# Kernel optimization log

Hardware: AMD Instinct MI355X
Metric: run time of the kernel (lower is better)

## Reference

```python
import jax, jax.numpy as jnp
import numpy as np

NUM_HEADS = 16
D_MODEL = 1024
DEPTH = D_MODEL // NUM_HEADS
THRESHOLD = 0.1
BATCH = 2
SEQ = 2048


def setup_inputs() -> dict:
    key = jax.random.key(0)
    ks = jax.random.split(key, 9)
    w_scale = 1.0 / np.sqrt(D_MODEL)
    Q = jax.random.normal(ks[0], (BATCH, SEQ, D_MODEL), dtype=jnp.float32)
    T = jax.random.normal(ks[1], (BATCH, SEQ, D_MODEL), dtype=jnp.float32)
    V = jax.random.normal(ks[2], (BATCH, SEQ, D_MODEL), dtype=jnp.float32)
    Wq = jax.random.normal(ks[3], (NUM_HEADS, D_MODEL, DEPTH), dtype=jnp.float32) * w_scale
    Wk = jax.random.normal(ks[4], (NUM_HEADS, D_MODEL, DEPTH), dtype=jnp.float32) * w_scale
    Wv = jax.random.normal(ks[5], (NUM_HEADS, D_MODEL, DEPTH), dtype=jnp.float32) * w_scale
    Wo = jax.random.normal(ks[6], (D_MODEL, D_MODEL), dtype=jnp.float32) * w_scale
    bq = jnp.zeros((NUM_HEADS, DEPTH), dtype=jnp.float32)
    bk = jnp.zeros((NUM_HEADS, DEPTH), dtype=jnp.float32)
    bv = jnp.zeros((NUM_HEADS, DEPTH), dtype=jnp.float32)
    bo = jnp.zeros((D_MODEL,), dtype=jnp.float32)
    return {"Q": Q, "T": T, "V": V, "Wq": Wq, "bq": bq, "Wk": Wk, "bk": bk,
            "Wv": Wv, "bv": bv, "Wo": Wo, "bo": bo}


def reference(Q, T, V, Wq, bq, Wk, bk, Wv, bv, Wo, bo):
    # Per-head projections (stacked over heads): [B,S,D] x [H,D,E] -> [B,H,S,E]
    q = jnp.einsum('bsd,hde->bhse', Q, Wq) + bq[None, :, None, :]
    k = jnp.einsum('bsd,hde->bhse', T, Wk) + bk[None, :, None, :]
    v = jnp.einsum('bsd,hde->bhse', V, Wv) + bv[None, :, None, :]

    # Raw scores (NOT pre-scaled): [B,H,S,S]
    scores = jnp.einsum('bhqe,bhke->bhqk', q, k)
    # tf.where(A>thr, A, -2**32 * cast(A>thr)) -> failing entries become 0
    scores = jnp.where(scores > THRESHOLD, scores, jnp.zeros((), scores.dtype))
    # M = 1 - lower_band(ones): +1 on strictly upper-triangular entries
    seq = scores.shape[-1]
    upper = jnp.triu(jnp.ones((seq, seq), dtype=scores.dtype), k=1)
    scores = (scores + upper) / jnp.sqrt(jnp.asarray(DEPTH, scores.dtype))

    attn = jax.nn.softmax(scores, axis=-1)
    out = jnp.einsum('bhqk,bhke->bhqe', attn, v)  # [B,H,S,E]
    B, H, S, E = out.shape
    concat = out.transpose(0, 2, 1, 3).reshape(B, S, H * E)  # [B,S,D]
    return concat @ Wo + bo
```

## Files before the change

kernel.cpp:

```cpp
#include <hip/hip_runtime.h>
#include <stdint.h>


typedef __attribute__((ext_vector_type(8))) short bf16x8;
typedef __attribute__((ext_vector_type(4))) float f32x4;

#define DEVFN static __device__ __forceinline__

static constexpr int S_ = 2048;
static constexpr int H_ = 16;

DEVFN unsigned short f2bf(float x) {
  union { float f; uint32_t u; } v; v.f = x;
  const uint32_t r = v.u + 0x7fffu + ((v.u >> 16) & 1u);
  return (unsigned short)(r >> 16);
}

DEVFN f32x4 fzero() { f32x4 v = {0.f, 0.f, 0.f, 0.f}; return v; }

union U8 { uint32_t u[4]; bf16x8 v; };

DEVFN void gld_lds16(const void* g, void* lds) {
  __builtin_amdgcn_global_load_lds(
      (const __attribute__((address_space(1))) void*)g,
      (__attribute__((address_space(3))) void*)lds, 16, 0, 0);
}

__global__ void prep_weights(const float* __restrict__ Wq, const float* __restrict__ Wk,
                             const float* __restrict__ Wv, const float* __restrict__ Wo,
                             unsigned short* __restrict__ dstBase) {
  const int z = blockIdx.z;
  const float* src = (z == 0) ? Wq : (z == 1) ? Wk : (z == 2) ? Wv : Wo;
  unsigned short* dst = dstBase + (size_t)z * (1024u * 1024u);
  const int idx = blockIdx.x * 256 + threadIdx.x;
  const int c = idx & 1023;
  const int d0 = (idx >> 10) << 3;
  unsigned short hv[8];
#pragma unroll
  for (int t = 0; t < 8; ++t) {
    const int d = d0 + t;
    const float v = (z < 3) ? src[(size_t)((c >> 6) * 1024 + d) * 64 + (c & 63)]
                            : src[(size_t)d * 1024 + c];
    hv[t] = f2bf(v);
  }
  *(uint4*)(dst + (size_t)c * 1024 + d0) = *(const uint4*)hv;
}

__global__ __launch_bounds__(256, 3)
void proj_gemm(const float* __restrict__ Qm, const float* __restrict__ Tm,
               const float* __restrict__ Vm, const unsigned short* __restrict__ Wt,
               const float* __restrict__ bq, const float* __restrict__ bk,
               const float* __restrict__ bv, unsigned short* __restrict__ qb,
               unsigned short* __restrict__ kb, unsigned short* __restrict__ vtb) {
  __shared__ float Af[2][128 * 32];
  __shared__ unsigned short Bt[2][128 * 32];

  const int tid = threadIdx.x;
  const int lane = tid & 63;
  const int w = tid >> 6;
  const int g = lane >> 4, c = lane & 15;
  const int wm = w >> 1, wn = w & 1;

  const int m0 = blockIdx.x * 128;
  const int proj = blockIdx.y >> 3;
  const int n0 = (blockIdx.y & 7) * 128;

  const float* Asrc = (proj == 0) ? Qm : (proj == 1) ? Tm : Vm;
  const unsigned short* W = Wt + (size_t)proj * (1024u * 1024u);

  f32x4 acc[4][4];
#pragma unroll
  for (int i = 0; i < 4; ++i)
#pragma unroll
    for (int j = 0; j < 4; ++j) acc[i][j] = fzero();

  const int arow = w * 8 + (lane >> 3);
  const int ach = lane & 7;
  const int brow = w * 16 + (lane >> 2);
  const int bch = lane & 3;

  auto stage = [&](int kt, int buf) {
#pragma unroll
    for (int u = 0; u < 4; ++u) {
      const int row = u * 32 + arow;
      const int ch = ach ^ (row & 7);
      gld_lds16(Asrc + (size_t)(m0 + row) * 1024 + kt * 32 + ch * 4,
                &Af[buf][(u * 32 + w * 8) * 32]);
    }
#pragma unroll
    for (int u = 0; u < 2; ++u) {
      const int row = u * 64 + brow;
      const int ch = bch ^ ((row >> 1) & 3);
      gld_lds16(W + (size_t)(n0 + row) * 1024 + kt * 32 + ch * 8,
                &Bt[buf][(u * 64 + w * 16) * 32]);
    }
  };

  stage(0, 0);
  __syncthreads();

  for (int kt = 0; kt < 32; ++kt) {
    const int buf = kt & 1;
    if (kt < 31) stage(kt + 1, buf ^ 1);

    bf16x8 af[4], bfr[4];
#pragma unroll
    for (int mi = 0; mi < 4; ++mi) {
      const int row = wm * 64 + mi * 16 + c;
      const int swz = row & 7;
      const float4 fa = *(const float4*)&Af[buf][row * 32 + ((2 * g) ^ swz) * 4];
      const float4 fb = *(const float4*)&Af[buf][row * 32 + ((2 * g + 1) ^ swz) * 4];
      U8 u8;
      asm("v_cvt_pk_bf16_f32 %0, %1, %2" : "=v"(u8.u[0]) : "v"(fa.x), "v"(fa.y));
      asm("v_cvt_pk_bf16_f32 %0, %1, %2" : "=v"(u8.u[1]) : "v"(fa.z), "v"(fa.w));
      asm("v_cvt_pk_bf16_f32 %0, %1, %2" : "=v"(u8.u[2]) : "v"(fb.x), "v"(fb.y));
      asm("v_cvt_pk_bf16_f32 %0, %1, %2" : "=v"(u8.u[3]) : "v"(fb.z), "v"(fb.w));
      af[mi] = u8.v;
    }
#pragma unroll
    for (int ni = 0; ni < 4; ++ni) {
      const int row = wn * 64 + ni * 16 + c;
      bfr[ni] = *(const bf16x8*)&Bt[buf][row * 32 + ((g ^ ((row >> 1) & 3))) * 8];
    }
#pragma unroll
    for (int mi = 0; mi < 4; ++mi)
#pragma unroll
      for (int ni = 0; ni < 4; ++ni)
        acc[mi][ni] = __builtin_amdgcn_mfma_f32_16x16x32_bf16(af[mi], bfr[ni],
                                                              acc[mi][ni], 0, 0, 0);
    __syncthreads();
  }

  const float* bias = (proj == 0) ? bq : (proj == 1) ? bk : bv;
  if (proj < 2) {
    unsigned short* dptr = (proj == 0) ? qb : kb;
#pragma unroll
    for (int ni = 0; ni < 4; ++ni) {
      const int colb = n0 + wn * 64 + ni * 16 + c;
      const float bc = bias[colb];
      const int hh = colb >> 6, e = colb & 63;
#pragma unroll
      for (int mi = 0; mi < 4; ++mi)
#pragma unroll
        for (int r = 0; r < 4; ++r) {
          const int row = m0 + wm * 64 + mi * 16 + g * 4 + r;
          const int bb = row >> 11, s = row & 2047;
          dptr[(((size_t)(bb * H_ + hh)) * S_ + s) * 64 + e] = f2bf(acc[mi][ni][r] + bc);
        }
    }
  } else {
#pragma unroll
    for (int ni = 0; ni < 4; ++ni) {
      const int colb = n0 + wn * 64 + ni * 16 + c;
      const float bc = bias[colb];
      const int hh = colb >> 6, e = colb & 63;
#pragma unroll
      for (int mi = 0; mi < 4; ++mi) {
        const int rowb = m0 + wm * 64 + mi * 16 + g * 4;
        const int bb = rowb >> 11, s0 = rowb & 2047;
        const float v0 = acc[mi][ni][0] + bc, v1 = acc[mi][ni][1] + bc;
        const float v2 = acc[mi][ni][2] + bc, v3 = acc[mi][ni][3] + bc;
        uint2 pk;
        asm("v_cvt_pk_bf16_f32 %0, %1, %2" : "=v"(pk.x) : "v"(v0), "v"(v1));
        asm("v_cvt_pk_bf16_f32 %0, %1, %2" : "=v"(pk.y) : "v"(v2), "v"(v3));
        *(uint2*)&vtb[(((size_t)(bb * H_ + hh)) * 64 + e) * S_ + s0] = pk;
      }
    }
  }
}

__global__ __launch_bounds__(256, 2)
void attn_kernel(const unsigned short* __restrict__ qb,
                 const unsigned short* __restrict__ kb,
                 const unsigned short* __restrict__ vtb,
                 unsigned short* __restrict__ att) {
  __shared__ unsigned short Kt[2][64 * 64];
  __shared__ unsigned short Vt[2][64 * 64];
  __shared__ unsigned short Pt[4][32 * 64];

  const int tid = threadIdx.x;
  const int lane = tid & 63;
  const int w = tid >> 6;
  const int g = lane >> 4, c = lane & 15;

  const int orig = blockIdx.x;
  const int logical = ((orig & 7) << 6) | (orig >> 3);
  const int qblk = logical & 15;
  const int bh = logical >> 4;
  const int hh = bh & 15, bz = bh >> 4;

  const int q0w = qblk * 128 + w * 32;
  const unsigned short* qh = qb + (size_t)bh * S_ * 64;
  const unsigned short* kh = kb + (size_t)bh * S_ * 64;
  const unsigned short* vh = vtb + (size_t)bh * 64 * S_;

  bf16x8 aq[2][2];
#pragma unroll
  for (int m = 0; m < 2; ++m)
#pragma unroll
    for (int t = 0; t < 2; ++t)
      aq[m][t] = *(const bf16x8*)&qh[(size_t)(q0w + m * 16 + c) * 64 + t * 32 + g * 8];

  bf16x8 onesB;
#pragma unroll
  for (int i = 0; i < 8; ++i) onesB[i] = (short)0x3F80;

  f32x4 O[2][4];
  f32x4 accL[2];
#pragma unroll
  for (int m = 0; m < 2; ++m) {
#pragma unroll
    for (int ne = 0; ne < 4; ++ne) O[m][ne] = fzero();
    accL[m] = fzero();
  }

  constexpr float L2E = 1.4426950408889634f;
  const float S2 = 0.125f * L2E;
  const float B2 = 0.125f * L2E;

  int kvOff[2][4], paOff[2][2], pwOff[2][4];
#pragma unroll
  for (int ks = 0; ks < 2; ++ks) {
#pragma unroll
    for (int mi = 0; mi < 4; ++mi) {
      const int row = mi * 16 + c;
      kvOff[ks][mi] = 2 * (row * 64 + ((ks * 4 + g) ^ (row & 7)) * 8);
    }
#pragma unroll
    for (int m = 0; m < 2; ++m)
      paOff[m][ks] = 2 * ((m * 16 + c) * 64 + ((ks * 4 + g) ^ (c & 7)) * 8);
  }
#pragma unroll
  for (int m = 0; m < 2; ++m)
#pragma unroll
    for (int mi = 0; mi < 4; ++mi)
      pwOff[m][mi] =
          2 * ((m * 16 + c) * 64 + ((2 * mi + (g >> 1)) ^ (c & 7)) * 8 + (g & 1) * 4);

  const int srow = w * 8 + (lane >> 3);
  const int sch = (lane & 7) ^ (srow & 7);
  const unsigned short* kS0 = kh + (size_t)srow * 64 + sch * 8;
  const unsigned short* kS1 = kh + (size_t)(32 + srow) * 64 + sch * 8;
  const unsigned short* vS0 = vh + (size_t)srow * S_ + sch * 8;
  const unsigned short* vS1 = vh + (size_t)(32 + srow) * S_ + sch * 8;

  {
    gld_lds16(kS0, &Kt[0][(w * 8) * 64]);
    gld_lds16(kS1, &Kt[0][(32 + w * 8) * 64]);
    gld_lds16(vS0, &Vt[0][(w * 8) * 64]);
    gld_lds16(vS1, &Vt[0][(32 + w * 8) * 64]);
  }
  __syncthreads();

#define ATTN_BODY(JT, CUR)                                                     \
  do {                                                                         \
    const int j0 = (JT) * 64;                                                  \
    if ((JT) < 31) {             \
      gld_lds16(kS0 + 4096, &Kt[CUR ^ 1][(w * 8) * 64]);                       \
      gld_lds16(kS1 + 4096, &Kt[CUR ^ 1][(32 + w * 8) * 64]);                  \
      gld_lds16(vS0 + 64, &Vt[CUR ^ 1][(w * 8) * 64]);                         \
      gld_lds16(vS1 + 64, &Vt[CUR ^ 1][(32 + w * 8) * 64]);                    \
      kS0 += 4096; kS1 += 4096; vS0 += 64; vS1 += 64;                          \
    }                                                                          \
    f32x4 sa[2][4];                                                            \
    _Pragma("unroll")                                                          \
    for (int m = 0; m < 2; ++m)                                                \
      _Pragma("unroll")                                                        \
      for (int mi = 0; mi < 4; ++mi) sa[m][mi] = fzero();                      \
    __builtin_amdgcn_s_setprio(1);                                             \
    _Pragma("unroll")                                                          \
    for (int ks = 0; ks < 2; ++ks)                                             \
      _Pragma("unroll")                                                        \
      for (int mi = 0; mi < 4; ++mi) {                                         \
        const bf16x8 ka =                                                      \
            *(const bf16x8*)((const char*)&Kt[CUR][0] + kvOff[ks][mi]);        \
        sa[0][mi] = __builtin_amdgcn_mfma_f32_16x16x32_bf16(ka, aq[0][ks],     \
                                                            sa[0][mi], 0, 0, 0);\
        sa[1][mi] = __builtin_amdgcn_mfma_f32_16x16x32_bf16(ka, aq[1][ks],     \
                                                            sa[1][mi], 0, 0, 0);\
      }                                                                        \
    __builtin_amdgcn_s_setprio(0);                                             \
    const bool allUp = (j0 >= q0w + 32);                                       \
    const bool noneUp = (j0 + 63 <= q0w);                                      \
    _Pragma("unroll")                                                          \
    for (int m = 0; m < 2; ++m) {                                              \
      const int iq = q0w + m * 16 + c;                                         \
      _Pragma("unroll")                                                        \
      for (int mi = 0; mi < 4; ++mi) {                                         \
        float pv[4];                                                           \
        if (allUp || noneUp) {                                                 \
          const float bb = allUp ? B2 : 0.f;                                   \
          _Pragma("unroll")                                                    \
          for (int r = 0; r < 4; ++r) {                                        \
            const float v = sa[m][mi][r];                                      \
            pv[r] = __builtin_amdgcn_exp2f(                                    \
                (v > 0.1f) ? __builtin_fmaf(v, S2, bb) : bb);                  \
          }                                                                    \
        } else {                                                               \
          _Pragma("unroll")                                                    \
          for (int r = 0; r < 4; ++r) {                                        \
            const float v = sa[m][mi][r];                                      \
            const float bb = (j0 + mi * 16 + g * 4 + r > iq) ? B2 : 0.f;       \
            pv[r] = __builtin_amdgcn_exp2f(                                    \
                (v > 0.1f) ? __builtin_fmaf(v, S2, bb) : bb);                  \
          }                                                                    \
        }                                                                      \
        uint2 d;                                                               \
        asm("v_cvt_pk_bf16_f32 %0, %1, %2"                                     \
            : "=v"(d.x) : "v"(pv[0]), "v"(pv[1]));                             \
        asm("v_cvt_pk_bf16_f32 %0, %1, %2"                                     \
            : "=v"(d.y) : "v"(pv[2]), "v"(pv[3]));                             \
        *(uint2*)((char*)&Pt[w][0] + pwOff[m][mi]) = d;                        \
      }                                                                        \
    }                                                                          \
    asm volatile("s_waitcnt lgkmcnt(0)" ::: "memory");                         \
    __builtin_amdgcn_sched_barrier(0);                                         \
    __builtin_amdgcn_s_setprio(1);                                             \
    _Pragma("unroll")                                                          \
    for (int ks = 0; ks < 2; ++ks) {                                           \
      const bf16x8 pa0 =                                                       \
          *(const bf16x8*)((const char*)&Pt[w][0] + paOff[0][ks]);             \
      const bf16x8 pa1 =                                                       \
          *(const bf16x8*)((const char*)&Pt[w][0] + paOff[1][ks]);             \
      accL[0] = __builtin_amdgcn_mfma_f32_16x16x32_bf16(pa0, onesB, accL[0],   \
                                                        0, 0, 0);              \
      accL[1] = __builtin_amdgcn_mfma_f32_16x16x32_bf16(pa1, onesB, accL[1],   \
                                                        0, 0, 0);              \
      _Pragma("unroll")                                                        \
      for (int ne = 0; ne < 4; ++ne) {                                         \
        const bf16x8 bv8 =                                                     \
            *(const bf16x8*)((const char*)&Vt[CUR][0] + kvOff[ks][ne]);        \
        O[0][ne] = __builtin_amdgcn_mfma_f32_16x16x32_bf16(pa0, bv8, O[0][ne], \
                                                           0, 0, 0);           \
        O[1][ne] = __builtin_amdgcn_mfma_f32_16x16x32_bf16(pa1, bv8, O[1][ne], \
                                                           0, 0, 0);           \
      }                                                                        \
    }                                                                          \
    __builtin_amdgcn_s_setprio(0);                                             \
    __syncthreads();                                                           \
  } while (0)

  for (int jt = 0; jt < 32; jt += 2) {
    ATTN_BODY(jt, 0);
    ATTN_BODY(jt + 1, 1);
  }
#undef ATTN_BODY

#pragma unroll
  for (int m = 0; m < 2; ++m)
#pragma unroll
    for (int r = 0; r < 4; ++r) {
      const float il = 1.f / accL[m][r];
      const int qg = q0w + m * 16 + g * 4 + r;
      const size_t ro = ((size_t)(bz * S_ + qg)) * 1024 + hh * 64;
#pragma unroll
      for (int ne = 0; ne < 4; ++ne)
        att[ro + ne * 16 + c] = f2bf(O[m][ne][r] * il);
    }
}

__global__ __launch_bounds__(256, 3)
void out_gemm(const unsigned short* __restrict__ att,
              const unsigned short* __restrict__ WoT,
              const float* __restrict__ bo, float* __restrict__ outp) {
  __shared__ unsigned short At[2][128 * 32];
  __shared__ unsigned short Bt[2][128 * 32];

  const int tid = threadIdx.x;
  const int lane = tid & 63;
  const int w = tid >> 6;
  const int g = lane >> 4, c = lane & 15;
  const int wm = w >> 1, wn = w & 1;
  const int m0 = blockIdx.x * 128;
  const int n0 = blockIdx.y * 128;

  f32x4 acc[4][4];
#pragma unroll
  for (int i = 0; i < 4; ++i)
#pragma unroll
    for (int j = 0; j < 4; ++j) acc[i][j] = fzero();

  const int srow = lane >> 2;
  const int sch = lane & 3;

  auto stage = [&](int kt, int buf) {
#pragma unroll
    for (int u = 0; u < 2; ++u) {
      const int row = u * 64 + w * 16 + srow;
      const int ch = sch ^ ((row >> 1) & 3);
      gld_lds16(att + (size_t)(m0 + row) * 1024 + kt * 32 + ch * 8,
                &At[buf][(u * 64 + w * 16) * 32]);
      gld_lds16(WoT + (size_t)(n0 + row) * 1024 + kt * 32 + ch * 8,
                &Bt[buf][(u * 64 + w * 16) * 32]);
    }
  };

  stage(0, 0);
  __syncthreads();

  for (int kt = 0; kt < 32; ++kt) {
    const int buf = kt & 1;
    if (kt < 31) stage(kt + 1, buf ^ 1);

    bf16x8 af[4], bfr[4];
#pragma unroll
    for (int mi = 0; mi < 4; ++mi) {
      const int row = wm * 64 + mi * 16 + c;
      af[mi] = *(const bf16x8*)&At[buf][row * 32 + ((g ^ ((row >> 1) & 3))) * 8];
    }
#pragma unroll
    for (int ni = 0; ni < 4; ++ni) {
      const int row = wn * 64 + ni * 16 + c;
      bfr[ni] = *(const bf16x8*)&Bt[buf][row * 32 + ((g ^ ((row >> 1) & 3))) * 8];
    }
#pragma unroll
    for (int mi = 0; mi < 4; ++mi)
#pragma unroll
      for (int ni = 0; ni < 4; ++ni)
        acc[mi][ni] = __builtin_amdgcn_mfma_f32_16x16x32_bf16(af[mi], bfr[ni],
                                                              acc[mi][ni], 0, 0, 0);
    __syncthreads();
  }

#pragma unroll
  for (int ni = 0; ni < 4; ++ni) {
    const int colb = n0 + wn * 64 + ni * 16 + c;
    const float bc = bo[colb];
#pragma unroll
    for (int mi = 0; mi < 4; ++mi)
#pragma unroll
      for (int r = 0; r < 4; ++r) {
        const int row = m0 + wm * 64 + mi * 16 + g * 4 + r;
        outp[(size_t)row * 1024 + colb] = acc[mi][ni][r] + bc;
      }
  }
}

extern "C" void kernel_launch(void* const* d_in, const int* in_sizes, int n_in,
                              void* d_out, int out_size, void* d_ws, size_t ws_size,
                              hipStream_t stream) {
  const float* Q  = (const float*)d_in[0];
  const float* T  = (const float*)d_in[1];
  const float* V  = (const float*)d_in[2];
  const float* Wq = (const float*)d_in[3];
  const float* bq = (const float*)d_in[4];
  const float* Wk = (const float*)d_in[5];
  const float* bk = (const float*)d_in[6];
  const float* Wv = (const float*)d_in[7];
  const float* bv = (const float*)d_in[8];
  const float* Wo = (const float*)d_in[9];
  const float* bo = (const float*)d_in[10];

  const size_t MB = 1024ull * 1024ull;
  if (ws_size < 40 * MB) return;

  uint8_t* ws = (uint8_t*)d_ws;
  unsigned short* Wt  = (unsigned short*)(ws);
  unsigned short* qb  = (unsigned short*)(ws + 8 * MB);
  unsigned short* kb  = (unsigned short*)(ws + 16 * MB);
  unsigned short* vtb = (unsigned short*)(ws + 24 * MB);
  unsigned short* attb = (unsigned short*)(ws + 32 * MB);

  prep_weights<<<dim3(512, 1, 4), 256, 0, stream>>>(Wq, Wk, Wv, Wo, Wt);
  proj_gemm<<<dim3(32, 24), 256, 0, stream>>>(Q, T, V, Wt, bq, bk, bv,
                                              qb, kb, vtb);
  attn_kernel<<<dim3(512), 256, 0, stream>>>(qb, kb, vtb, attb);
  out_gemm<<<dim3(32, 8), 256, 0, stream>>>(attb, Wt + 3ull * 1024ull * 1024ull,
                                            bo, (float*)d_out);
}
```

Before: 133.1 us.

## Pre-convert activations to bf16 and enlarge projection GEMM tiles with triple buffering

Adds a convert_a kernel that turns Q/T/V from fp32 into bf16 ahead of time, writing into d_out and the attention scratch buffer, so the projection GEMM no longer loads fp32 tiles or converts them inside the inner loop. The projection GEMM now uses 256x256 tiles with 512 threads, a three-stage LDS pipeline with partial vmcnt waits, and s_setprio around the MFMAs. This halves A-side LDS and global traffic in the GEMM and improves reuse, at the cost of an extra kernel launch, an extra pass over the activations, larger register and LDS use, and fewer blocks (192) on the GPU.

```diff
diff --git a/kernel.cpp b/kernel.cpp
--- a/kernel.cpp
+++ b/kernel.cpp
@@ -17,8 +17,6 @@
 }
 
 DEVFN f32x4 fzero() { f32x4 v = {0.f, 0.f, 0.f, 0.f}; return v; }
-
-union U8 { uint32_t u[4]; bf16x8 v; };
 
 DEVFN void gld_lds16(const void* g, void* lds) {
   __builtin_amdgcn_global_load_lds(
@@ -46,90 +44,120 @@
   *(uint4*)(dst + (size_t)c * 1024 + d0) = *(const uint4*)hv;
 }
 
-__global__ __launch_bounds__(256, 3)
-void proj_gemm(const float* __restrict__ Qm, const float* __restrict__ Tm,
-               const float* __restrict__ Vm, const unsigned short* __restrict__ Wt,
+__global__ void convert_a(const float* __restrict__ Qm, const float* __restrict__ Tm,
+                          const float* __restrict__ Vm, unsigned short* __restrict__ aq,
+                          unsigned short* __restrict__ at2, unsigned short* __restrict__ av) {
+  const int z = blockIdx.z;
+  const float* s = (z == 0) ? Qm : (z == 1) ? Tm : Vm;
+  unsigned short* d = (z == 0) ? aq : (z == 1) ? at2 : av;
+  const size_t i = ((size_t)blockIdx.x * 256 + threadIdx.x) * 8;
+  const float4 f0 = *(const float4*)(s + i);
+  const float4 f1 = *(const float4*)(s + i + 4);
+  uint32_t d0, d1, d2, d3;
+  asm("v_cvt_pk_bf16_f32 %0, %1, %2" : "=v"(d0) : "v"(f0.x), "v"(f0.y));
+  asm("v_cvt_pk_bf16_f32 %0, %1, %2" : "=v"(d1) : "v"(f0.z), "v"(f0.w));
+  asm("v_cvt_pk_bf16_f32 %0, %1, %2" : "=v"(d2) : "v"(f1.x), "v"(f1.y));
+  asm("v_cvt_pk_bf16_f32 %0, %1, %2" : "=v"(d3) : "v"(f1.z), "v"(f1.w));
+  uint4 o; o.x = d0; o.y = d1; o.z = d2; o.w = d3;
+  *(uint4*)(d + i) = o;
+}
+
+__global__ __launch_bounds__(512, 2)
+void proj_gemm(const unsigned short* __restrict__ Aq,
+               const unsigned short* __restrict__ At2,
+               const unsigned short* __restrict__ Av,
+               const unsigned short* __restrict__ Wt,
                const float* __restrict__ bq, const float* __restrict__ bk,
                const float* __restrict__ bv, unsigned short* __restrict__ qb,
                unsigned short* __restrict__ kb, unsigned short* __restrict__ vtb) {
-  __shared__ float Af[2][128 * 32];
-  __shared__ unsigned short Bt[2][128 * 32];
+  __shared__ unsigned short At[3][256 * 32];
+  __shared__ unsigned short Bt[3][256 * 32];
 
   const int tid = threadIdx.x;
   const int lane = tid & 63;
   const int w = tid >> 6;
   const int g = lane >> 4, c = lane & 15;
-  const int wm = w >> 1, wn = w & 1;
-
-  const int m0 = blockIdx.x * 128;
-  const int proj = blockIdx.y >> 3;
-  const int n0 = (blockIdx.y & 7) * 128;
-
-  const float* Asrc = (proj == 0) ? Qm : (proj == 1) ? Tm : Vm;
+  const int wm = w >> 2;
+  const int wn = w & 3;
+
+  const int m0 = blockIdx.x * 256;
+  const int proj = blockIdx.y >> 2;
+  const int n0 = (blockIdx.y & 3) * 256;
+
+  const unsigned short* Abf = (proj == 0) ? Aq : (proj == 1) ? At2 : Av;
   const unsigned short* W = Wt + (size_t)proj * (1024u * 1024u);
 
-  f32x4 acc[4][4];
-#pragma unroll
-  for (int i = 0; i < 4; ++i)
+  f32x4 acc[8][4];
+#pragma unroll
+  for (int i = 0; i < 8; ++i)
 #pragma unroll
     for (int j = 0; j < 4; ++j) acc[i][j] = fzero();
 
-  const int arow = w * 8 + (lane >> 3);
-  const int ach = lane & 7;
-  const int brow = w * 16 + (lane >> 2);
-  const int bch = lane & 3;
-
-  auto stage = [&](int kt, int buf) {
-#pragma unroll
-    for (int u = 0; u < 4; ++u) {
-      const int row = u * 32 + arow;
-      const int ch = ach ^ (row & 7);
-      gld_lds16(Asrc + (size_t)(m0 + row) * 1024 + kt * 32 + ch * 4,
-                &Af[buf][(u * 32 + w * 8) * 32]);
-    }
-#pragma unroll
-    for (int u = 0; u < 2; ++u) {
-      const int row = u * 64 + brow;
-      const int ch = bch ^ ((row >> 1) & 3);
-      gld_lds16(W + (size_t)(n0 + row) * 1024 + kt * 32 + ch * 8,
-                &Bt[buf][(u * 64 + w * 16) * 32]);
-    }
-  };
-
-  stage(0, 0);
-  __syncthreads();
-
-  for (int kt = 0; kt < 32; ++kt) {
-    const int buf = kt & 1;
-    if (kt < 31) stage(kt + 1, buf ^ 1);
-
-    bf16x8 af[4], bfr[4];
-#pragma unroll
-    for (int mi = 0; mi < 4; ++mi) {
-      const int row = wm * 64 + mi * 16 + c;
-      const int swz = row & 7;
-      const float4 fa = *(const float4*)&Af[buf][row * 32 + ((2 * g) ^ swz) * 4];
-      const float4 fb = *(const float4*)&Af[buf][row * 32 + ((2 * g + 1) ^ swz) * 4];
-      U8 u8;
-      asm("v_cvt_pk_bf16_f32 %0, %1, %2" : "=v"(u8.u[0]) : "v"(fa.x), "v"(fa.y));
-      asm("v_cvt_pk_bf16_f32 %0, %1, %2" : "=v"(u8.u[1]) : "v"(fa.z), "v"(fa.w));
-      asm("v_cvt_pk_bf16_f32 %0, %1, %2" : "=v"(u8.u[2]) : "v"(fb.x), "v"(fb.y));
-      asm("v_cvt_pk_bf16_f32 %0, %1, %2" : "=v"(u8.u[3]) : "v"(fb.z), "v"(fb.w));
-      af[mi] = u8.v;
-    }
-#pragma unroll
-    for (int ni = 0; ni < 4; ++ni) {
-      const int row = wn * 64 + ni * 16 + c;
-      bfr[ni] = *(const bf16x8*)&Bt[buf][row * 32 + ((g ^ ((row >> 1) & 3))) * 8];
-    }
-#pragma unroll
-    for (int mi = 0; mi < 4; ++mi)
-#pragma unroll
-      for (int ni = 0; ni < 4; ++ni)
-        acc[mi][ni] = __builtin_amdgcn_mfma_f32_16x16x32_bf16(af[mi], bfr[ni],
-                                                              acc[mi][ni], 0, 0, 0);
-    __syncthreads();
-  }
+  const int srow = w * 16 + (lane >> 2);
+  const int schB = lane & 3;
+
+#define PSTAGE(KT, BUF)                                                        \
+  do {                                                                         \
+    _Pragma("unroll")                                                          \
+    for (int u = 0; u < 2; ++u) {                                              \
+      const int row = u * 128 + srow;                                          \
+      const int ch = schB ^ ((row >> 1) & 3);                                  \
+      gld_lds16(Abf + (size_t)(m0 + row) * 1024 + (KT) * 32 + ch * 8,          \
+                &At[BUF][(u * 128 + w * 16) * 32]);                            \
+    }                                                                          \
+    _Pragma("unroll")                                                          \
+    for (int u = 0; u < 2; ++u) {                                              \
+      const int row = u * 128 + srow;                                          \
+      const int ch = schB ^ ((row >> 1) & 3);                                  \
+      gld_lds16(W + (size_t)(n0 + row) * 1024 + (KT) * 32 + ch * 8,            \
+                &Bt[BUF][(u * 128 + w * 16) * 32]);                            \
+    }                                                                          \
+  } while (0)
+
+#define PBODY(KT, CUR, STG)                                                    \
+  do {                                                                         \
+    if ((KT) + 2 < 32) PSTAGE((KT) + 2, STG);                                  \
+    bf16x8 af[8], bfr[4];                                                      \
+    _Pragma("unroll")                                                          \
+    for (int mi = 0; mi < 8; ++mi) {                                           \
+      const int row = wm * 128 + mi * 16 + c;                                  \
+      af[mi] = *(const bf16x8*)&At[CUR][row * 32 +                             \
+                                        ((g ^ ((row >> 1) & 3))) * 8];         \
+    }                                                                          \
+    _Pragma("unroll")                                                          \
+    for (int ni = 0; ni < 4; ++ni) {                                           \
+      const int row = wn * 64 + ni * 16 + c;                                   \
+      bfr[ni] = *(const bf16x8*)&Bt[CUR][row * 32 +                            \
+                                         ((g ^ ((row >> 1) & 3))) * 8];        \
+    }                                                                          \
+    __builtin_amdgcn_s_setprio(1);                                             \
+    _Pragma("unroll")                                                          \
+    for (int mi = 0; mi < 8; ++mi)                                             \
+      _Pragma("unroll")                                                        \
+      for (int ni = 0; ni < 4; ++ni)                                           \
+        acc[mi][ni] = __builtin_amdgcn_mfma_f32_16x16x32_bf16(                 \
+            af[mi], bfr[ni], acc[mi][ni], 0, 0, 0);                            \
+    __builtin_amdgcn_s_setprio(0);                                             \
+    asm volatile("s_waitcnt vmcnt(4)" ::: "memory");                           \
+    __builtin_amdgcn_s_barrier();                                              \
+    asm volatile("" ::: "memory");                                             \
+  } while (0)
+
+  PSTAGE(0, 0);
+  PSTAGE(1, 1);
+  asm volatile("s_waitcnt vmcnt(4)" ::: "memory");
+  __builtin_amdgcn_s_barrier();
+  asm volatile("" ::: "memory");
+
+  for (int kb = 0; kb < 30; kb += 3) {
+    PBODY(kb + 0, 0, 2);
+    PBODY(kb + 1, 1, 0);
+    PBODY(kb + 2, 2, 1);
+  }
+  PBODY(30, 0, 2);
+  PBODY(31, 1, 0);
+#undef PBODY
+#undef PSTAGE
 
   const float* bias = (proj == 0) ? bq : (proj == 1) ? bk : bv;
   if (proj < 2) {
@@ -140,10 +168,10 @@
       const float bc = bias[colb];
       const int hh = colb >> 6, e = colb & 63;
 #pragma unroll
-      for (int mi = 0; mi < 4; ++mi)
+      for (int mi = 0; mi < 8; ++mi)
 #pragma unroll
         for (int r = 0; r < 4; ++r) {
-          const int row = m0 + wm * 64 + mi * 16 + g * 4 + r;
+          const int row = m0 + wm * 128 + mi * 16 + g * 4 + r;
           const int bb = row >> 11, s = row & 2047;
           dptr[(((size_t)(bb * H_ + hh)) * S_ + s) * 64 + e] = f2bf(acc[mi][ni][r] + bc);
         }
@@ -155,8 +183,8 @@
       const float bc = bias[colb];
       const int hh = colb >> 6, e = colb & 63;
 #pragma unroll
-      for (int mi = 0; mi < 4; ++mi) {
-        const int rowb = m0 + wm * 64 + mi * 16 + g * 4;
+      for (int mi = 0; mi < 8; ++mi) {
+        const int rowb = m0 + wm * 128 + mi * 16 + g * 4;
         const int bb = rowb >> 11, s0 = rowb & 2047;
         const float v0 = acc[mi][ni][0] + bc, v1 = acc[mi][ni][1] + bc;
         const float v2 = acc[mi][ni][2] + bc, v3 = acc[mi][ni][3] + bc;
@@ -255,7 +283,7 @@
 #define ATTN_BODY(JT, CUR)                                                     \
   do {                                                                         \
     const int j0 = (JT) * 64;                                                  \
-    if ((JT) < 31) {             \
+    if ((JT) < 31) {                                                           \
       gld_lds16(kS0 + 4096, &Kt[CUR ^ 1][(w * 8) * 64]);                       \
       gld_lds16(kS1 + 4096, &Kt[CUR ^ 1][(32 + w * 8) * 64]);                  \
       gld_lds16(vS0 + 64, &Vt[CUR ^ 1][(w * 8) * 64]);                         \
@@ -461,8 +489,13 @@
   unsigned short* vtb = (unsigned short*)(ws + 24 * MB);
   unsigned short* attb = (unsigned short*)(ws + 32 * MB);
 
+  unsigned short* aQ = (unsigned short*)d_out;
+  unsigned short* aT = aQ + 4ull * 1024ull * 1024ull;
+  unsigned short* aV = attb;
+
   prep_weights<<<dim3(512, 1, 4), 256, 0, stream>>>(Wq, Wk, Wv, Wo, Wt);
-  proj_gemm<<<dim3(32, 24), 256, 0, stream>>>(Q, T, V, Wt, bq, bk, bv,
+  convert_a<<<dim3(2048, 1, 3), 256, 0, stream>>>(Q, T, V, aQ, aT, aV);
+  proj_gemm<<<dim3(16, 12), 512, 0, stream>>>(aQ, aT, aV, Wt, bq, bk, bv,
                                               qb, kb, vtb);
   attn_kernel<<<dim3(512), 256, 0, stream>>>(qb, kb, vtb, attb);
   out_gemm<<<dim3(32, 8), 256, 0, stream>>>(attb, Wt + 3ull * 1024ull * 1024ull,
```

New measurement: 146.4 us. +10.0%, slower.
